# Kernel tuning notes

Hardware: AMD Instinct MI355X
Metric: run time of the kernel (lower is better)

## Reference

```python
import jax, jax.numpy as jnp
import numpy as np

B = 16          # batch
DF = 1536       # dinov2 feature dim
D = 1024        # projected dim (32*32)
V = 6890        # SMPL vertices (hard-coded in DECO)
PD = 256        # vertex positional-embedding dim
HID = 512       # feature_transform hidden dim
C = 133         # semantic contact classes


def setup_inputs() -> dict:
    key = jax.random.key(0)
    ks = jax.random.split(key, 16)
    s = 0.02
    n = lambda k, shp: s * jax.random.normal(k, shp, dtype=jnp.float32)
    return {
        "features": jax.random.normal(ks[0], (B, DF), dtype=jnp.float32),
        "W_scene": n(ks[1], (DF, D)), "b_scene": jnp.zeros((D,), jnp.float32),
        "W_contact": n(ks[2], (DF, D)), "b_contact": jnp.zeros((D,), jnp.float32),
        "Wq": n(ks[3], (D, D)), "Wk": n(ks[4], (D, D)),
        "Wv": n(ks[5], (D, D)), "Wo": n(ks[6], (D, D)),
        "W_cls": n(ks[7], (D, V)), "b_cls": jnp.zeros((V,), jnp.float32),
        "pos_emb": n(ks[8], (V, PD)),
        "W_ft1": n(ks[9], (D + PD, HID)), "b_ft1": jnp.zeros((HID,), jnp.float32),
        "W_ft2": n(ks[10], (HID, C)), "b_ft2": jnp.zeros((C,), jnp.float32),
    }


def reference(features, W_scene, b_scene, W_contact, b_contact,
              Wq, Wk, Wv, Wo, W_cls, b_cls, pos_emb,
              W_ft1, b_ft1, W_ft2, b_ft2):
    b = features.shape[0]
    # projectors (dinov2 branch)
    sem = features @ W_scene + b_scene          # [B, D]
    part = features @ W_contact + b_contact     # [B, D]
    # cross attention over seq-len-1 tokens: q from sem, k/v from part
    q = (sem @ Wq)[:, None, :]                  # [B, 1, D]
    k = (part @ Wk)[:, None, :]
    v = (part @ Wv)[:, None, :]
    scores = jnp.einsum('bqd,bkd->bqk', q, k) / jnp.sqrt(jnp.float32(D))
    w = jax.nn.softmax(scores, axis=-1)
    att = jnp.einsum('bqk,bkd->bqd', w, v) @ Wo  # [B, 1, D]
    # per-vertex contact probability
    cont = jax.nn.sigmoid(att[:, 0, :] @ W_cls + b_cls)  # [B, V]
    # shared semantic classifier: the torch code loops over batches, does
    # nonzero() on (cont > 0.5), gathers pos embeddings for contact vertices,
    # runs feature_transform, and scatters into zeros(B, C, V). The masked
    # vectorized form below computes identical values.
    mask = cont > 0.5                           # [B, V] (int constant wrt grad)
    att_bv = jnp.broadcast_to(att, (b, V, D))   # att[b] repeated per vertex
    pos_bv = jnp.broadcast_to(pos_emb[None], (b, V, PD))
    combined = jnp.concatenate([att_bv, pos_bv], axis=-1)   # [B, V, D+PD]
    h = jax.nn.relu(combined @ W_ft1 + b_ft1)   # [B, V, HID]
    preds = h @ W_ft2 + b_ft2                   # [B, V, C]
    semantic_cont = jnp.where(mask[:, None, :],
                              jnp.transpose(preds, (0, 2, 1)),
                              jnp.float32(0.0))  # [B, C, V]
    return (cont, semantic_cont)
```

## Files before the change

kernel.cpp:

```cpp
#include <hip/hip_runtime.h>
#include <hip/hip_bf16.h>

#define B_   16
#define DF_  1536
#define D_   1024
#define V_   6890
#define PD_  256
#define HID_ 512
#define C_   133
#define VPAD 6912
#define CPAD 144

typedef short short8 __attribute__((ext_vector_type(8)));
typedef float float4_ __attribute__((ext_vector_type(4)));
typedef unsigned short ushort_t;

#define MFMA16 __builtin_amdgcn_mfma_f32_16x16x32_bf16

__device__ __forceinline__ float b2f(ushort_t u) {
  union { unsigned int i; float f; } x;
  x.i = ((unsigned int)u) << 16;
  return x.f;
}
__device__ __forceinline__ ushort_t f2b(float f) {
  union { float f; unsigned int i; } x;
  x.f = f;
  unsigned int r = (x.i + 0x7fffu + ((x.i >> 16) & 1u)) >> 16;
  return (ushort_t)r;
}
__device__ __forceinline__ unsigned int f22u(float h0, float h1) {
  __hip_bfloat162 hb = __float22bfloat162_rn(make_float2(h0, h1));
  unsigned int u;
  __builtin_memcpy(&u, &hb, sizeof(u));
  return u;
}

__global__ __launch_bounds__(256) void k_gemv_fA(const float* __restrict__ A,
                                                 const float* __restrict__ W,
                                                 const float* __restrict__ bias,
                                                 double* __restrict__ outd,
                                                 float* __restrict__ outf,
                                                 int K, int N) {
  __shared__ double sA[DF_];
  int b = blockIdx.y;
  for (int i = threadIdx.x; i < K; i += 256) sA[i] = (double)A[b * K + i];
  __syncthreads();
  int jl = threadIdx.x & 15, ks = threadIdx.x >> 4;
  int j  = blockIdx.x * 16 + jl;
  int klen = K >> 4;
  const double* Ar = sA + ks * klen;
  const float*  Wp = W + (size_t)(ks * klen) * N + j;
  double acc = 0.0;
#pragma unroll 8
  for (int kk = 0; kk < klen; ++kk)
    acc += Ar[kk] * (double)Wp[(size_t)kk * N];
  __shared__ double red[16][16];
  red[ks][jl] = acc;
  __syncthreads();
  if (threadIdx.x < 16) {
    int jj = blockIdx.x * 16 + threadIdx.x;
    double s = 0.0;
#pragma unroll
    for (int q = 0; q < 16; ++q) s += red[q][threadIdx.x];
    if (bias) s += (double)bias[jj];
    if (outd) outd[b * N + jj] = s;
    if (outf) outf[b * N + jj] = (float)s;
  }
}

__global__ __launch_bounds__(256) void k_gemv_dA(const double* __restrict__ A,
                                                 const float* __restrict__ W,
                                                 const float* __restrict__ bias,
                                                 double* __restrict__ outd,
                                                 float* __restrict__ outf,
                                                 int K, int N) {
  __shared__ double sA[D_];
  int b = blockIdx.y;
  for (int i = threadIdx.x; i < K; i += 256) sA[i] = A[b * K + i];
  __syncthreads();
  int jl = threadIdx.x & 15, ks = threadIdx.x >> 4;
  int j  = blockIdx.x * 16 + jl;
  int klen = K >> 4;
  const double* Ar = sA + ks * klen;
  const float*  Wp = W + (size_t)(ks * klen) * N + j;
  double acc = 0.0;
#pragma unroll 8
  for (int kk = 0; kk < klen; ++kk)
    acc += Ar[kk] * (double)Wp[(size_t)kk * N];
  __shared__ double red[16][16];
  red[ks][jl] = acc;
  __syncthreads();
  if (threadIdx.x < 16) {
    int jj = blockIdx.x * 16 + threadIdx.x;
    double s = 0.0;
#pragma unroll
    for (int q = 0; q < 16; ++q) s += red[q][threadIdx.x];
    if (bias) s += (double)bias[jj];
    if (outd) outd[b * N + jj] = s;
    if (outf) outf[b * N + jj] = (float)s;
  }
}

__global__ __launch_bounds__(256) void k_cont(const double* __restrict__ att,
                                              const float* __restrict__ Wcls,
                                              const float* __restrict__ bcls,
                                              unsigned char* __restrict__ maskb,
                                              float* __restrict__ out0) {
  int vl = threadIdx.x & 15, ks = threadIdx.x >> 4;
  int v  = blockIdx.x * 16 + vl;
  int vc = v < V_ ? v : V_ - 1;
  double acc[B_];
#pragma unroll
  for (int b = 0; b < B_; ++b) acc[b] = 0.0;
  int k0 = ks * 64;
#pragma unroll 8
  for (int kk = 0; kk < 64; ++kk) {
    int k = k0 + kk;
    double w = (double)Wcls[(size_t)k * V_ + vc];
#pragma unroll
    for (int b = 0; b < B_; ++b) acc[b] += att[b * D_ + k] * w;
  }
  __shared__ double red[16][B_][16];
#pragma unroll
  for (int b = 0; b < B_; ++b) red[ks][b][vl] = acc[b];
  __syncthreads();
  int b = threadIdx.x >> 4;
  double s = 0.0;
#pragma unroll
  for (int q = 0; q < 16; ++q) s += red[q][b][vl];
  if (v < V_) {
    s += (double)bcls[v];
    maskb[b * V_ + v] = (s > 0.0) ? 1 : 0;
    out0[b * V_ + v] = (float)(1.0 / (1.0 + exp(-s)));
  }
}

__global__ __launch_bounds__(256) void k_prep(const float* __restrict__ Wft2,
                                              const float* __restrict__ Wft1,
                                              const float* __restrict__ pos,
                                              ushort_t* __restrict__ WT,
                                              ushort_t* __restrict__ WbT,
                                              ushort_t* __restrict__ PB) {
  int i = blockIdx.x * 256 + threadIdx.x;
  if (i < CPAD * HID_) {
    int c = i >> 9, k = i & (HID_ - 1);
    WT[i] = (c < C_) ? f2b(Wft2[(size_t)k * C_ + c]) : (ushort_t)0;
    return;
  }
  i -= CPAD * HID_;
  if (i < HID_ * PD_) {
    int k = i & (HID_ - 1), pd = i >> 9;
    WbT[(size_t)k * PD_ + pd] = f2b(Wft1[(size_t)(D_ + pd) * HID_ + k]);
    return;
  }
  i -= HID_ * PD_;
  if (i < V_ * PD_) PB[i] = f2b(pos[i]);
}

__global__ __launch_bounds__(256) void k_pproj(const ushort_t* __restrict__ PB,
                                               const ushort_t* __restrict__ WbT,
                                               ushort_t* __restrict__ PP) {
  int wave = threadIdx.x >> 6, lane = threadIdx.x & 63;
  int q = lane >> 4, l15 = lane & 15;
  int m0 = blockIdx.x * 64 + wave * 16;
  int n0 = blockIdx.y * 64;
  int vc = m0 + l15; vc = vc < V_ ? vc : V_ - 1;
  const ushort_t* pb = PB + (size_t)vc * PD_;
  float4_ acc[4] = {};
#pragma unroll 2
  for (int kt = 0; kt < 8; ++kt) {
    int jb = kt * 32 + q * 8;
    short8 a = *(const short8*)(pb + jb);
#pragma unroll
    for (int nf = 0; nf < 4; ++nf) {
      int n = n0 + nf * 16 + l15;
      short8 bfr = *(const short8*)(WbT + (size_t)n * PD_ + jb);
      acc[nf] = MFMA16(a, bfr, acc[nf], 0, 0, 0);
    }
  }
  int v0w = m0 + q * 4;
#pragma unroll
  for (int nf = 0; nf < 4; ++nf)
#pragma unroll
    for (int r = 0; r < 4; ++r)
      PP[(size_t)(v0w + r) * HID_ + (n0 + nf * 16 + l15)] = f2b(acc[nf][r]);
}

__global__ __launch_bounds__(256, 2) void k_main(const ushort_t* __restrict__ WT,
                                                 const ushort_t* __restrict__ PP,
                                                 const float* __restrict__ attproj,
                                                 const unsigned char* __restrict__ maskb,
                                                 const float* __restrict__ bft2,
                                                 float* __restrict__ out1) {
  __shared__ ushort_t swt[2][CPAD * 32];
  __shared__ float attp[2][HID_];
  int b0 = blockIdx.y * 2;
  int wave = threadIdx.x >> 6, lane = threadIdx.x & 63;
  int q = lane >> 4, l15 = lane & 15;
  int vbase = blockIdx.x * 128 + wave * 32;

  for (int i = threadIdx.x; i < 2 * HID_; i += 256)
    attp[i >> 9][i & (HID_ - 1)] = attproj[(b0 + (i >> 9)) * HID_ + (i & (HID_ - 1))];

  auto stage = [&](int kt, int buf) {
#pragma unroll
    for (int ii = 0; ii < 3; ++ii) {
      int i = ii * 256 + threadIdx.x;
      if (i < 576) {
        int row = i >> 2, seg = i & 3;
        *(short8*)&swt[buf][row * 32 + seg * 8] =
            *(const short8*)(WT + (size_t)row * HID_ + kt * 32 + seg * 8);
      }
    }
  };
  stage(0, 0);

  const ushort_t* pbase0 = PP + (size_t)(vbase + l15) * HID_;
  const ushort_t* pbase1 = PP + (size_t)(vbase + 16 + l15) * HID_;
  short8 pcur[2];
  pcur[0] = *(const short8*)(pbase0 + q * 8);
  pcur[1] = *(const short8*)(pbase1 + q * 8);
  __syncthreads();

  float4_ acc[2][9][2] = {};
  for (int kt = 0; kt < 16; ++kt) {
    int buf = kt & 1;
    int kb = kt * 32 + q * 8;
    if (kt < 15) stage(kt + 1, buf ^ 1);
    short8 pnext[2] = {pcur[0], pcur[1]};
    if (kt < 15) {
      pnext[0] = *(const short8*)(pbase0 + kb + 32);
      pnext[1] = *(const short8*)(pbase1 + kb + 32);
    }
    float pf[2][8];
#pragma unroll
    for (int nf = 0; nf < 2; ++nf)
#pragma unroll
      for (int jj = 0; jj < 8; ++jj)
        pf[nf][jj] = b2f((ushort_t)pcur[nf][jj]);
    float af[2][8];
#pragma unroll
    for (int bb = 0; bb < 2; ++bb) {
      float4_ a0 = *(const float4_*)&attp[bb][kb];
      float4_ a1 = *(const float4_*)&attp[bb][kb + 4];
#pragma unroll
      for (int e = 0; e < 4; ++e) { af[bb][e] = a0[e]; af[bb][4 + e] = a1[e]; }
    }
    short8 bfr[2][2];
#pragma unroll
    for (int bb = 0; bb < 2; ++bb)
#pragma unroll
      for (int nf = 0; nf < 2; ++nf) {
        unsigned int uu[4];
#pragma unroll
        for (int jj = 0; jj < 8; jj += 2) {
          float h0 = af[bb][jj]     + pf[nf][jj];
          float h1 = af[bb][jj + 1] + pf[nf][jj + 1];
          h0 = h0 > 0.f ? h0 : 0.f;
          h1 = h1 > 0.f ? h1 : 0.f;
          uu[jj >> 1] = f22u(h0, h1);
        }
        __builtin_memcpy(&bfr[bb][nf], uu, 16);
      }
#pragma unroll
    for (int mt = 0; mt < 9; ++mt) {
      short8 a = *(const short8*)&swt[buf][(mt * 16 + l15) * 32 + q * 8];
      acc[0][mt][0] = MFMA16(a, bfr[0][0], acc[0][mt][0], 0, 0, 0);
      acc[0][mt][1] = MFMA16(a, bfr[0][1], acc[0][mt][1], 0, 0, 0);
      acc[1][mt][0] = MFMA16(a, bfr[1][0], acc[1][mt][0], 0, 0, 0);
      acc[1][mt][1] = MFMA16(a, bfr[1][1], acc[1][mt][1], 0, 0, 0);
    }
    pcur[0] = pnext[0];
    pcur[1] = pnext[1];
    __syncthreads();
  }

  bool mk[2][2];
  int  nn[2];
#pragma unroll
  for (int nf = 0; nf < 2; ++nf) {
    int n = vbase + nf * 16 + l15;
    nn[nf] = n;
    int ncl = n < V_ ? n : V_ - 1;
    mk[0][nf] = (n < V_) && (maskb[(b0 + 0) * V_ + ncl] != 0);
    mk[1][nf] = (n < V_) && (maskb[(b0 + 1) * V_ + ncl] != 0);
  }
#pragma unroll
  for (int bb = 0; bb < 2; ++bb) {
    float* ob = out1 + (size_t)(b0 + bb) * C_ * V_;
#pragma unroll
    for (int mt = 0; mt < 9; ++mt)
#pragma unroll
      for (int r = 0; r < 4; ++r) {
        int c = mt * 16 + q * 4 + r;
        if (c < C_) {
          float bias = bft2[c];
#pragma unroll
          for (int nf = 0; nf < 2; ++nf)
            if (nn[nf] < V_) {
              float val = mk[bb][nf] ? acc[bb][mt][nf][r] + bias : 0.f;
              ob[(size_t)c * V_ + nn[nf]] = val;
            }
        }
      }
  }
}

extern "C" void kernel_launch(void* const* d_in, const int* in_sizes, int n_in,
                              void* d_out, int out_size, void* d_ws, size_t ws_size,
                              hipStream_t stream) {
  const float* features  = (const float*)d_in[0];
  const float* W_contact = (const float*)d_in[3];
  const float* b_contact = (const float*)d_in[4];
  const float* Wv        = (const float*)d_in[7];
  const float* Wo        = (const float*)d_in[8];
  const float* W_cls     = (const float*)d_in[9];
  const float* b_cls     = (const float*)d_in[10];
  const float* pos_emb   = (const float*)d_in[11];
  const float* W_ft1     = (const float*)d_in[12];
  const float* b_ft1     = (const float*)d_in[13];
  const float* W_ft2     = (const float*)d_in[14];
  const float* b_ft2     = (const float*)d_in[15];

  char* ws = (char*)d_ws;
  double*        part  = (double*)(ws);
  unsigned char* maskb = (unsigned char*)(ws);
  double*        vv    = (double*)(ws + 131072);
  double*        att   = (double*)(ws + 262144);
  float*         attpj = (float*)(ws + 393216);
  ushort_t*      wt    = (ushort_t*)(ws + 425984);
  ushort_t*      wbt   = (ushort_t*)(ws + 573440);
  ushort_t*      pp    = (ushort_t*)(ws + 835584);
  ushort_t*      pb    = (ushort_t*)(ws + 7913472);

  float* out0 = (float*)d_out;
  float* out1 = out0 + (size_t)B_ * V_;

  k_prep<<<7690, 256, 0, stream>>>(W_ft2, W_ft1, pos_emb, wt, wbt, pb);
  k_pproj<<<dim3(108, 8), 256, 0, stream>>>(pb, wbt, pp);
  k_gemv_fA<<<dim3(64, 16), 256, 0, stream>>>(features, W_contact, b_contact, part, nullptr, DF_, D_);
  k_gemv_dA<<<dim3(64, 16), 256, 0, stream>>>(part, Wv, nullptr, vv, nullptr, D_, D_);
  k_gemv_dA<<<dim3(64, 16), 256, 0, stream>>>(vv, Wo, nullptr, att, nullptr, D_, D_);
  k_gemv_dA<<<dim3(32, 16), 256, 0, stream>>>(att, W_ft1, b_ft1, nullptr, attpj, D_, HID_);
  k_cont<<<432, 256, 0, stream>>>(att, W_cls, b_cls, maskb, out0);
  k_main<<<dim3(54, 8), 256, 0, stream>>>(wt, pp, attpj, maskb, b_ft2, out1);
}
```

Measured before the change: 266.3 us.

## Fuse GEMV chain into cooperative kernel, stage pos in LDS, retile main kernel

The weight-prep work and the four dependent GEMVs plus the contact classifier now run in one cooperative kernel, using grid-wide syncs in place of separate launches. The pos-embedding bf16 conversion moves into k_pproj, which converts into swizzled LDS, so the PB intermediate buffer is gone. k_main is retiled to 64 vertices per block with a K-step of 64, a swizzled LDS layout for WT and a 3-blocks-per-SM occupancy hint. The intent is to cut launch overhead and intermediate global traffic. The risks are the cost of grid syncs and underused CUs in the serial GEMV phases, since only 512 blocks run there.

```diff
diff --git a/kernel.cpp b/kernel.cpp
--- a/kernel.cpp
+++ b/kernel.cpp
@@ -1,5 +1,8 @@
 #include <hip/hip_runtime.h>
 #include <hip/hip_bf16.h>
+#include <hip/hip_cooperative_groups.h>
+
+namespace cg = cooperative_groups;
 
 #define B_   16
 #define DF_  1536
@@ -35,142 +38,135 @@
   return u;
 }
 
-__global__ __launch_bounds__(256) void k_gemv_fA(const float* __restrict__ A,
-                                                 const float* __restrict__ W,
-                                                 const float* __restrict__ bias,
-                                                 double* __restrict__ outd,
-                                                 float* __restrict__ outf,
-                                                 int K, int N) {
-  __shared__ double sA[DF_];
-  int b = blockIdx.y;
-  for (int i = threadIdx.x; i < K; i += 256) sA[i] = (double)A[b * K + i];
+__device__ void gemv_pair(const float* __restrict__ A32,
+                          const double* __restrict__ A64,
+                          const float* __restrict__ W,
+                          const float* __restrict__ bias,
+                          double* __restrict__ outd, float* __restrict__ outf,
+                          int K, int N, int b, int jb0, int njb, double* sh) {
+  double* sA = sh;
+  double* red = sh + 2560;
+  for (int i = threadIdx.x; i < K; i += 256)
+    sA[i] = A32 ? (double)A32[(size_t)b * K + i] : A64[(size_t)b * K + i];
   __syncthreads();
   int jl = threadIdx.x & 15, ks = threadIdx.x >> 4;
-  int j  = blockIdx.x * 16 + jl;
   int klen = K >> 4;
-  const double* Ar = sA + ks * klen;
-  const float*  Wp = W + (size_t)(ks * klen) * N + j;
-  double acc = 0.0;
+  for (int t = 0; t < njb; ++t) {
+    int jb = jb0 + t;
+    int j = jb * 16 + jl;
+    const double* Ar = sA + ks * klen;
+    const float* Wp = W + (size_t)(ks * klen) * N + j;
+    double acc = 0.0;
 #pragma unroll 8
-  for (int kk = 0; kk < klen; ++kk)
-    acc += Ar[kk] * (double)Wp[(size_t)kk * N];
-  __shared__ double red[16][16];
-  red[ks][jl] = acc;
-  __syncthreads();
-  if (threadIdx.x < 16) {
-    int jj = blockIdx.x * 16 + threadIdx.x;
+    for (int kk = 0; kk < klen; ++kk)
+      acc += Ar[kk] * (double)Wp[(size_t)kk * N];
+    red[ks * 16 + jl] = acc;
+    __syncthreads();
+    if (threadIdx.x < 16) {
+      double s = 0.0;
+#pragma unroll
+      for (int q2 = 0; q2 < 16; ++q2) s += red[q2 * 16 + threadIdx.x];
+      int jj = jb * 16 + threadIdx.x;
+      if (bias) s += (double)bias[jj];
+      if (outd) outd[(size_t)b * N + jj] = s;
+      if (outf) outf[(size_t)b * N + jj] = (float)s;
+    }
+    __syncthreads();
+  }
+}
+
+__global__ __launch_bounds__(256, 4) void k_chain(
+    const float* __restrict__ features, const float* __restrict__ W_contact,
+    const float* __restrict__ b_contact, const float* __restrict__ Wv,
+    const float* __restrict__ Wo, const float* __restrict__ Wcls,
+    const float* __restrict__ bcls, const float* __restrict__ Wft1,
+    const float* __restrict__ bft1, const float* __restrict__ Wft2,
+    double* __restrict__ part, double* __restrict__ vv,
+    double* __restrict__ att, float* __restrict__ attpj,
+    unsigned char* __restrict__ maskb, ushort_t* __restrict__ wt,
+    ushort_t* __restrict__ wbt, float* __restrict__ out0) {
+  __shared__ double sh[4096];
+  int bid = blockIdx.x, tid = threadIdx.x;
+
+  for (int i = bid * 256 + tid; i < CPAD * HID_ + HID_ * PD_; i += 512 * 256) {
+    if (i < CPAD * HID_) {
+      int c = i >> 9, k = i & (HID_ - 1);
+      wt[i] = (c < C_) ? f2b(Wft2[(size_t)k * C_ + c]) : (ushort_t)0;
+    } else {
+      int j = i - CPAD * HID_;
+      int k = j & (HID_ - 1), pd = j >> 9;
+      wbt[(size_t)k * PD_ + pd] = f2b(Wft1[(size_t)(D_ + pd) * HID_ + k]);
+    }
+  }
+
+  int b = bid >> 5;
+  int jb0 = (2 * bid) & 63;
+  gemv_pair(features, nullptr, W_contact, b_contact, part, nullptr, DF_, D_, b, jb0, 2, sh);
+  cg::this_grid().sync();
+  gemv_pair(nullptr, part, Wv, nullptr, vv, nullptr, D_, D_, b, jb0, 2, sh);
+  cg::this_grid().sync();
+  gemv_pair(nullptr, vv, Wo, nullptr, att, nullptr, D_, D_, b, jb0, 2, sh);
+  cg::this_grid().sync();
+  gemv_pair(nullptr, att, Wft1, bft1, nullptr, attpj, D_, HID_, b, bid & 31, 1, sh);
+
+  if (bid < 432) {
+    int vl = tid & 15, ks = tid >> 4;
+    int v = bid * 16 + vl;
+    int vc = v < V_ ? v : V_ - 1;
+    double acc[B_];
+#pragma unroll
+    for (int q2 = 0; q2 < B_; ++q2) acc[q2] = 0.0;
+    int k0 = ks * 64;
+#pragma unroll 8
+    for (int kk = 0; kk < 64; ++kk) {
+      int k = k0 + kk;
+      double w = (double)Wcls[(size_t)k * V_ + vc];
+#pragma unroll
+      for (int q2 = 0; q2 < B_; ++q2) acc[q2] += att[q2 * D_ + k] * w;
+    }
+    double* red = sh;
+#pragma unroll
+    for (int q2 = 0; q2 < B_; ++q2) red[(ks * 16 + q2) * 16 + vl] = acc[q2];
+    __syncthreads();
+    int bb2 = tid >> 4;
     double s = 0.0;
 #pragma unroll
-    for (int q = 0; q < 16; ++q) s += red[q][threadIdx.x];
-    if (bias) s += (double)bias[jj];
-    if (outd) outd[b * N + jj] = s;
-    if (outf) outf[b * N + jj] = (float)s;
-  }
-}
-
-__global__ __launch_bounds__(256) void k_gemv_dA(const double* __restrict__ A,
-                                                 const float* __restrict__ W,
-                                                 const float* __restrict__ bias,
-                                                 double* __restrict__ outd,
-                                                 float* __restrict__ outf,
-                                                 int K, int N) {
-  __shared__ double sA[D_];
-  int b = blockIdx.y;
-  for (int i = threadIdx.x; i < K; i += 256) sA[i] = A[b * K + i];
-  __syncthreads();
-  int jl = threadIdx.x & 15, ks = threadIdx.x >> 4;
-  int j  = blockIdx.x * 16 + jl;
-  int klen = K >> 4;
-  const double* Ar = sA + ks * klen;
-  const float*  Wp = W + (size_t)(ks * klen) * N + j;
-  double acc = 0.0;
-#pragma unroll 8
-  for (int kk = 0; kk < klen; ++kk)
-    acc += Ar[kk] * (double)Wp[(size_t)kk * N];
-  __shared__ double red[16][16];
-  red[ks][jl] = acc;
-  __syncthreads();
-  if (threadIdx.x < 16) {
-    int jj = blockIdx.x * 16 + threadIdx.x;
-    double s = 0.0;
-#pragma unroll
-    for (int q = 0; q < 16; ++q) s += red[q][threadIdx.x];
-    if (bias) s += (double)bias[jj];
-    if (outd) outd[b * N + jj] = s;
-    if (outf) outf[b * N + jj] = (float)s;
-  }
-}
-
-__global__ __launch_bounds__(256) void k_cont(const double* __restrict__ att,
-                                              const float* __restrict__ Wcls,
-                                              const float* __restrict__ bcls,
-                                              unsigned char* __restrict__ maskb,
-                                              float* __restrict__ out0) {
-  int vl = threadIdx.x & 15, ks = threadIdx.x >> 4;
-  int v  = blockIdx.x * 16 + vl;
-  int vc = v < V_ ? v : V_ - 1;
-  double acc[B_];
-#pragma unroll
-  for (int b = 0; b < B_; ++b) acc[b] = 0.0;
-  int k0 = ks * 64;
-#pragma unroll 8
-  for (int kk = 0; kk < 64; ++kk) {
-    int k = k0 + kk;
-    double w = (double)Wcls[(size_t)k * V_ + vc];
-#pragma unroll
-    for (int b = 0; b < B_; ++b) acc[b] += att[b * D_ + k] * w;
-  }
-  __shared__ double red[16][B_][16];
-#pragma unroll
-  for (int b = 0; b < B_; ++b) red[ks][b][vl] = acc[b];
-  __syncthreads();
-  int b = threadIdx.x >> 4;
-  double s = 0.0;
-#pragma unroll
-  for (int q = 0; q < 16; ++q) s += red[q][b][vl];
-  if (v < V_) {
-    s += (double)bcls[v];
-    maskb[b * V_ + v] = (s > 0.0) ? 1 : 0;
-    out0[b * V_ + v] = (float)(1.0 / (1.0 + exp(-s)));
-  }
-}
-
-__global__ __launch_bounds__(256) void k_prep(const float* __restrict__ Wft2,
-                                              const float* __restrict__ Wft1,
-                                              const float* __restrict__ pos,
-                                              ushort_t* __restrict__ WT,
-                                              ushort_t* __restrict__ WbT,
-                                              ushort_t* __restrict__ PB) {
-  int i = blockIdx.x * 256 + threadIdx.x;
-  if (i < CPAD * HID_) {
-    int c = i >> 9, k = i & (HID_ - 1);
-    WT[i] = (c < C_) ? f2b(Wft2[(size_t)k * C_ + c]) : (ushort_t)0;
-    return;
-  }
-  i -= CPAD * HID_;
-  if (i < HID_ * PD_) {
-    int k = i & (HID_ - 1), pd = i >> 9;
-    WbT[(size_t)k * PD_ + pd] = f2b(Wft1[(size_t)(D_ + pd) * HID_ + k]);
-    return;
-  }
-  i -= HID_ * PD_;
-  if (i < V_ * PD_) PB[i] = f2b(pos[i]);
-}
-
-__global__ __launch_bounds__(256) void k_pproj(const ushort_t* __restrict__ PB,
+    for (int q2 = 0; q2 < 16; ++q2) s += red[(q2 * 16 + bb2) * 16 + vl];
+    if (v < V_) {
+      s += (double)bcls[v];
+      maskb[bb2 * V_ + v] = (s > 0.0) ? 1 : 0;
+      out0[bb2 * V_ + v] = (float)(1.0 / (1.0 + exp(-s)));
+    }
+  }
+}
+
+__global__ __launch_bounds__(256) void k_pproj(const float* __restrict__ pos,
                                                const ushort_t* __restrict__ WbT,
                                                ushort_t* __restrict__ PP) {
+  __shared__ ushort_t pb_lds[64 * 256];
   int wave = threadIdx.x >> 6, lane = threadIdx.x & 63;
   int q = lane >> 4, l15 = lane & 15;
-  int m0 = blockIdx.x * 64 + wave * 16;
+  int vblk = blockIdx.x * 64;
   int n0 = blockIdx.y * 64;
-  int vc = m0 + l15; vc = vc < V_ ? vc : V_ - 1;
-  const ushort_t* pb = PB + (size_t)vc * PD_;
+
+  for (int i = threadIdx.x; i < 64 * 128; i += 256) {
+    int v = i >> 7, e2 = i & 127;
+    int vc = vblk + v; vc = vc < V_ ? vc : V_ - 1;
+    const float* sp = pos + (size_t)vc * PD_ + e2 * 2;
+    unsigned int u = f22u(sp[0], sp[1]);
+    int bsw = (e2 * 4) ^ ((v & 7) << 4);
+    *(unsigned int*)((char*)pb_lds + v * 512 + bsw) = u;
+  }
+  __syncthreads();
+
+  int m0 = wave * 16;
   float4_ acc[4] = {};
 #pragma unroll 2
   for (int kt = 0; kt < 8; ++kt) {
     int jb = kt * 32 + q * 8;
-    short8 a = *(const short8*)(pb + jb);
+    int row = m0 + l15;
+    int bsw = (jb * 2) ^ ((row & 7) << 4);
+    short8 a = *(const short8*)((const char*)pb_lds + row * 512 + bsw);
 #pragma unroll
     for (int nf = 0; nf < 4; ++nf) {
       int n = n0 + nf * 16 + l15;
@@ -178,7 +174,7 @@
       acc[nf] = MFMA16(a, bfr, acc[nf], 0, 0, 0);
     }
   }
-  int v0w = m0 + q * 4;
+  int v0w = vblk + m0 + q * 4;
 #pragma unroll
   for (int nf = 0; nf < 4; ++nf)
 #pragma unroll
@@ -186,105 +182,97 @@
       PP[(size_t)(v0w + r) * HID_ + (n0 + nf * 16 + l15)] = f2b(acc[nf][r]);
 }
 
-__global__ __launch_bounds__(256, 2) void k_main(const ushort_t* __restrict__ WT,
-                                                 const ushort_t* __restrict__ PP,
-                                                 const float* __restrict__ attproj,
-                                                 const unsigned char* __restrict__ maskb,
-                                                 const float* __restrict__ bft2,
-                                                 float* __restrict__ out1) {
-  __shared__ ushort_t swt[2][CPAD * 32];
+__global__ __launch_bounds__(256, 3) void k_main(
+    const ushort_t* __restrict__ WT, const ushort_t* __restrict__ PP,
+    const float* __restrict__ attproj, const unsigned char* __restrict__ maskb,
+    const float* __restrict__ bft2, float* __restrict__ out1) {
+  __shared__ ushort_t swt[2][CPAD * 64];
   __shared__ float attp[2][HID_];
   int b0 = blockIdx.y * 2;
   int wave = threadIdx.x >> 6, lane = threadIdx.x & 63;
   int q = lane >> 4, l15 = lane & 15;
-  int vbase = blockIdx.x * 128 + wave * 32;
+  int vbase = blockIdx.x * 64 + wave * 16;
 
   for (int i = threadIdx.x; i < 2 * HID_; i += 256)
-    attp[i >> 9][i & (HID_ - 1)] = attproj[(b0 + (i >> 9)) * HID_ + (i & (HID_ - 1))];
+    attp[i >> 9][i & (HID_ - 1)] =
+        attproj[(b0 + (i >> 9)) * HID_ + (i & (HID_ - 1))];
 
   auto stage = [&](int kt, int buf) {
 #pragma unroll
-    for (int ii = 0; ii < 3; ++ii) {
+    for (int ii = 0; ii < 5; ++ii) {
       int i = ii * 256 + threadIdx.x;
-      if (i < 576) {
-        int row = i >> 2, seg = i & 3;
-        *(short8*)&swt[buf][row * 32 + seg * 8] =
-            *(const short8*)(WT + (size_t)row * HID_ + kt * 32 + seg * 8);
+      if (i < 1152) {
+        int row = i >> 3, seg = i & 7;
+        short8 w = *(const short8*)(WT + (size_t)row * HID_ + kt * 64 + seg * 8);
+        int bsw = (seg * 16) ^ ((row & 7) << 4);
+        *(short8*)((char*)swt[buf] + row * 128 + bsw) = w;
       }
     }
   };
+
+  const ushort_t* pbase = PP + (size_t)(vbase + l15) * HID_;
+  short8 pcur[2], pnext[2];
+  pcur[0] = *(const short8*)(pbase + q * 8);
+  pcur[1] = *(const short8*)(pbase + 32 + q * 8);
   stage(0, 0);
-
-  const ushort_t* pbase0 = PP + (size_t)(vbase + l15) * HID_;
-  const ushort_t* pbase1 = PP + (size_t)(vbase + 16 + l15) * HID_;
-  short8 pcur[2];
-  pcur[0] = *(const short8*)(pbase0 + q * 8);
-  pcur[1] = *(const short8*)(pbase1 + q * 8);
   __syncthreads();
 
-  float4_ acc[2][9][2] = {};
-  for (int kt = 0; kt < 16; ++kt) {
+  float4_ acc[2][9] = {};
+  for (int kt = 0; kt < 8; ++kt) {
     int buf = kt & 1;
-    int kb = kt * 32 + q * 8;
-    if (kt < 15) stage(kt + 1, buf ^ 1);
-    short8 pnext[2] = {pcur[0], pcur[1]};
-    if (kt < 15) {
-      pnext[0] = *(const short8*)(pbase0 + kb + 32);
-      pnext[1] = *(const short8*)(pbase1 + kb + 32);
-    }
-    float pf[2][8];
-#pragma unroll
-    for (int nf = 0; nf < 2; ++nf)
-#pragma unroll
-      for (int jj = 0; jj < 8; ++jj)
-        pf[nf][jj] = b2f((ushort_t)pcur[nf][jj]);
-    float af[2][8];
-#pragma unroll
-    for (int bb = 0; bb < 2; ++bb) {
-      float4_ a0 = *(const float4_*)&attp[bb][kb];
-      float4_ a1 = *(const float4_*)&attp[bb][kb + 4];
-#pragma unroll
-      for (int e = 0; e < 4; ++e) { af[bb][e] = a0[e]; af[bb][4 + e] = a1[e]; }
+    if (kt < 7) stage(kt + 1, buf ^ 1);
+    pnext[0] = pcur[0]; pnext[1] = pcur[1];
+    if (kt < 7) {
+      pnext[0] = *(const short8*)(pbase + (kt + 1) * 64 + q * 8);
+      pnext[1] = *(const short8*)(pbase + (kt + 1) * 64 + 32 + q * 8);
     }
     short8 bfr[2][2];
 #pragma unroll
-    for (int bb = 0; bb < 2; ++bb)
-#pragma unroll
-      for (int nf = 0; nf < 2; ++nf) {
+    for (int ss = 0; ss < 2; ++ss) {
+      int kb = kt * 64 + ss * 32 + q * 8;
+      float pf[8];
+#pragma unroll
+      for (int jj = 0; jj < 8; ++jj) pf[jj] = b2f((ushort_t)pcur[ss][jj]);
+#pragma unroll
+      for (int bb = 0; bb < 2; ++bb) {
+        float4_ a0 = *(const float4_*)&attp[bb][kb];
+        float4_ a1 = *(const float4_*)&attp[bb][kb + 4];
+        float af[8];
+#pragma unroll
+        for (int e = 0; e < 4; ++e) { af[e] = a0[e]; af[4 + e] = a1[e]; }
         unsigned int uu[4];
 #pragma unroll
         for (int jj = 0; jj < 8; jj += 2) {
-          float h0 = af[bb][jj]     + pf[nf][jj];
-          float h1 = af[bb][jj + 1] + pf[nf][jj + 1];
+          float h0 = af[jj] + pf[jj];
+          float h1 = af[jj + 1] + pf[jj + 1];
           h0 = h0 > 0.f ? h0 : 0.f;
           h1 = h1 > 0.f ? h1 : 0.f;
           uu[jj >> 1] = f22u(h0, h1);
         }
-        __builtin_memcpy(&bfr[bb][nf], uu, 16);
+        __builtin_memcpy(&bfr[bb][ss], uu, 16);
       }
-#pragma unroll
-    for (int mt = 0; mt < 9; ++mt) {
-      short8 a = *(const short8*)&swt[buf][(mt * 16 + l15) * 32 + q * 8];
-      acc[0][mt][0] = MFMA16(a, bfr[0][0], acc[0][mt][0], 0, 0, 0);
-      acc[0][mt][1] = MFMA16(a, bfr[0][1], acc[0][mt][1], 0, 0, 0);
-      acc[1][mt][0] = MFMA16(a, bfr[1][0], acc[1][mt][0], 0, 0, 0);
-      acc[1][mt][1] = MFMA16(a, bfr[1][1], acc[1][mt][1], 0, 0, 0);
-    }
-    pcur[0] = pnext[0];
-    pcur[1] = pnext[1];
+    }
+#pragma unroll
+    for (int ss = 0; ss < 2; ++ss) {
+      int cb = ss * 64 + q * 16;
+#pragma unroll
+      for (int mt = 0; mt < 9; ++mt) {
+        int row = mt * 16 + l15;
+        short8 a = *(const short8*)((const char*)swt[buf] + row * 128 +
+                                    (cb ^ ((row & 7) << 4)));
+        acc[0][mt] = MFMA16(a, bfr[0][ss], acc[0][mt], 0, 0, 0);
+        acc[1][mt] = MFMA16(a, bfr[1][ss], acc[1][mt], 0, 0, 0);
+      }
+    }
+    pcur[0] = pnext[0]; pcur[1] = pnext[1];
     __syncthreads();
   }
 
-  bool mk[2][2];
-  int  nn[2];
-#pragma unroll
-  for (int nf = 0; nf < 2; ++nf) {
-    int n = vbase + nf * 16 + l15;
-    nn[nf] = n;
-    int ncl = n < V_ ? n : V_ - 1;
-    mk[0][nf] = (n < V_) && (maskb[(b0 + 0) * V_ + ncl] != 0);
-    mk[1][nf] = (n < V_) && (maskb[(b0 + 1) * V_ + ncl] != 0);
-  }
+  int n = vbase + l15;
+  int ncl = n < V_ ? n : V_ - 1;
+  bool mk[2];
+  mk[0] = (n < V_) && (maskb[(b0 + 0) * V_ + ncl] != 0);
+  mk[1] = (n < V_) && (maskb[(b0 + 1) * V_ + ncl] != 0);
 #pragma unroll
   for (int bb = 0; bb < 2; ++bb) {
     float* ob = out1 + (size_t)(b0 + bb) * C_ * V_;
@@ -293,14 +281,9 @@
 #pragma unroll
       for (int r = 0; r < 4; ++r) {
         int c = mt * 16 + q * 4 + r;
-        if (c < C_) {
-          float bias = bft2[c];
-#pragma unroll
-          for (int nf = 0; nf < 2; ++nf)
-            if (nn[nf] < V_) {
-              float val = mk[bb][nf] ? acc[bb][mt][nf][r] + bias : 0.f;
-              ob[(size_t)c * V_ + nn[nf]] = val;
-            }
+        if (c < C_ && n < V_) {
+          float val = mk[bb] ? acc[bb][mt][r] + bft2[c] : 0.f;
+          ob[(size_t)c * V_ + n] = val;
         }
       }
   }
@@ -324,24 +307,24 @@
 
   char* ws = (char*)d_ws;
   double*        part  = (double*)(ws);
-  unsigned char* maskb = (unsigned char*)(ws);
   double*        vv    = (double*)(ws + 131072);
   double*        att   = (double*)(ws + 262144);
   float*         attpj = (float*)(ws + 393216);
-  ushort_t*      wt    = (ushort_t*)(ws + 425984);
-  ushort_t*      wbt   = (ushort_t*)(ws + 573440);
-  ushort_t*      pp    = (ushort_t*)(ws + 835584);
-  ushort_t*      pb    = (ushort_t*)(ws + 7913472);
+  unsigned char* maskb = (unsigned char*)(ws + 425984);
+  ushort_t*      wt    = (ushort_t*)(ws + 536576);
+  ushort_t*      wbt   = (ushort_t*)(ws + 684032);
+  ushort_t*      pp    = (ushort_t*)(ws + 946176);
 
   float* out0 = (float*)d_out;
   float* out1 = out0 + (size_t)B_ * V_;
 
-  k_prep<<<7690, 256, 0, stream>>>(W_ft2, W_ft1, pos_emb, wt, wbt, pb);
-  k_pproj<<<dim3(108, 8), 256, 0, stream>>>(pb, wbt, pp);
-  k_gemv_fA<<<dim3(64, 16), 256, 0, stream>>>(features, W_contact, b_contact, part, nullptr, DF_, D_);
-  k_gemv_dA<<<dim3(64, 16), 256, 0, stream>>>(part, Wv, nullptr, vv, nullptr, D_, D_);
-  k_gemv_dA<<<dim3(64, 16), 256, 0, stream>>>(vv, Wo, nullptr, att, nullptr, D_, D_);
-  k_gemv_dA<<<dim3(32, 16), 256, 0, stream>>>(att, W_ft1, b_ft1, nullptr, attpj, D_, HID_);
-  k_cont<<<432, 256, 0, stream>>>(att, W_cls, b_cls, maskb, out0);
-  k_main<<<dim3(54, 8), 256, 0, stream>>>(wt, pp, attpj, maskb, b_ft2, out1);
-}
+  void* kargs[] = {
+      (void*)&features, (void*)&W_contact, (void*)&b_contact, (void*)&Wv,
+      (void*)&Wo, (void*)&W_cls, (void*)&b_cls, (void*)&W_ft1, (void*)&b_ft1,
+      (void*)&W_ft2, (void*)&part, (void*)&vv, (void*)&att, (void*)&attpj,
+      (void*)&maskb, (void*)&wt, (void*)&wbt, (void*)&out0};
+  hipLaunchCooperativeKernel((void*)k_chain, dim3(512), dim3(256), kargs, 0,
+                             stream);
+  k_pproj<<<dim3(108, 8), 256, 0, stream>>>(pos_emb, wbt, pp);
+  k_main<<<dim3(108, 8), 256, 0, stream>>>(wt, pp, attpj, maskb, b_ft2, out1);
+}
```

New measurement: 495.4 us. 1.86x slower.
